# Performance work log

Measured on AMD Instinct MI355X. Metric: run time of the kernel, lower is better.

The kernel has to match this reference:

```python
import jax, jax.numpy as jnp
import numpy as np

N, E, F_IN, HID, C = 50000, 800000, 512, 256, 64
K, ALPHA = 10, 0.1


def setup_inputs() -> dict:
    key = jax.random.key(0)
    ks = jax.random.split(key, 6)
    x = jax.random.normal(ks[0], (N, F_IN), dtype=jnp.float32)
    edge_index = jax.random.randint(ks[1], (2, E), 0, N, dtype=jnp.int64)
    W1 = jax.random.normal(ks[2], (F_IN, HID), dtype=jnp.float32) / np.sqrt(F_IN)
    b1 = jnp.zeros((HID,), dtype=jnp.float32)
    W2 = jax.random.normal(ks[3], (HID, C), dtype=jnp.float32) / np.sqrt(HID)
    b2 = jnp.zeros((C,), dtype=jnp.float32)
    return {"x": x, "W1": W1, "b1": b1, "W2": W2, "b2": b2, "edge_index": edge_index}


def reference(x, W1, b1, W2, b2, edge_index):
    # MLP (dropout is identity in eval mode)
    h = jax.nn.relu(x @ W1 + b1)
    h = h @ W2 + b2  # [N, C]

    n = x.shape[0]
    self_loops = jnp.arange(n, dtype=edge_index.dtype)
    row = jnp.concatenate([edge_index[0], self_loops])  # source nodes
    col = jnp.concatenate([edge_index[1], self_loops])  # target nodes

    # GCN symmetric normalization with self-loops (PyG gcn_norm)
    deg = jax.ops.segment_sum(jnp.ones_like(col, dtype=h.dtype), col, num_segments=n)
    dinv = jnp.where(deg > 0, jax.lax.rsqrt(jnp.maximum(deg, 1e-12)), 0.0)
    norm = (dinv[row] * dinv[col])[:, None]  # [E+N, 1]

    x0 = h

    def step(z, _):
        msg = z[row] * norm                                    # gather + scale
        agg = jax.ops.segment_sum(msg, col, num_segments=n)    # scatter-add
        return (1.0 - ALPHA) * agg + ALPHA * x0, None

    z, _ = jax.lax.scan(step, x0, None, length=K)
    return z
```

## Files before the change

### kernel.cpp

```cpp
#include <hip/hip_runtime.h>

#define N_NODES 50000
#define N_EDGES 800000
#define F_INDIM 512
#define HID     256
#define N_CLS   64
#define K_STEPS 10
#define ALPHA_V 0.1f

#define NPB 28
#define NPW 7
#define ECAP 1536

typedef __attribute__((ext_vector_type(8))) short short8;
typedef __attribute__((ext_vector_type(4))) float f32x4;
typedef __attribute__((ext_vector_type(4))) unsigned short ushort4v;

__device__ __forceinline__ unsigned short f2bf(float f) {
  unsigned u = __builtin_bit_cast(unsigned, f);
  unsigned r = (u + 0x7fffu + ((u >> 16) & 1u)) >> 16;
  return (unsigned short)r;
}
__device__ __forceinline__ float bflo(unsigned g) {
  return __builtin_bit_cast(float, g << 16);
}
__device__ __forceinline__ float bfhi(unsigned g) {
  return __builtin_bit_cast(float, g & 0xffff0000u);
}

#define GLOAD_LDS16(g, l)                                                        \
  __builtin_amdgcn_global_load_lds(                                              \
      (const __attribute__((address_space(1))) unsigned int*)(g),                \
      (__attribute__((address_space(3))) unsigned int*)(l), 16, 0, 0)

__global__ void detect_kernel(const int* __restrict__ eb, int* __restrict__ flag) {
  __shared__ int any;
  if (threadIdx.x == 0) any = 0;
  __syncthreads();
  for (int j = threadIdx.x; j < 1024; j += 256) {
    if (eb[2 * j + 1] != 0) atomicOr(&any, 1);
  }
  __syncthreads();
  if (threadIdx.x == 0) flag[0] = any ? 0 : 1;
}

__global__ void count_kernel(const int* __restrict__ eb, const int* __restrict__ flagp,
                             int* __restrict__ cnt) {
  int e = blockIdx.x * 256 + threadIdx.x;
  if (e >= N_EDGES) return;
  int sh = flagp[0];
  int c = eb[((size_t)(N_EDGES + e)) << sh];
  atomicAdd(&cnt[c], 1);
}

__global__ void scan1_kernel(const int* __restrict__ cnt, int* __restrict__ ptr,
                             int* __restrict__ bsum) {
  __shared__ int sm[256];
  int t = threadIdx.x;
  int i = blockIdx.x * 256 + t;
  int v = (i < N_NODES) ? cnt[i] : 0;
  sm[t] = v;
  __syncthreads();
  for (int off = 1; off < 256; off <<= 1) {
    int x = sm[t];
    if (t >= off) x += sm[t - off];
    __syncthreads();
    sm[t] = x;
    __syncthreads();
  }
  int incl = sm[t];
  if (i < N_NODES) ptr[i] = incl - v;
  if (t == 255) bsum[blockIdx.x] = incl;
}

__global__ void scan2_kernel(int* __restrict__ bsum, int nblk) {
  __shared__ int sm[256];
  int t = threadIdx.x;
  int v = (t < nblk) ? bsum[t] : 0;
  sm[t] = v;
  __syncthreads();
  for (int off = 1; off < 256; off <<= 1) {
    int x = sm[t];
    if (t >= off) x += sm[t - off];
    __syncthreads();
    sm[t] = x;
    __syncthreads();
  }
  int incl = sm[t];
  if (t < nblk) bsum[t] = incl - v;
}

__global__ void scan3_kernel(int* __restrict__ ptr, const int* __restrict__ bsum) {
  int i = blockIdx.x * 256 + threadIdx.x;
  if (i < N_NODES) ptr[i] += bsum[i >> 8];
  if (i == 0) ptr[N_NODES] = N_EDGES;
}

__global__ void dinv_kernel(const int* __restrict__ cnt, const int* __restrict__ ptr,
                            float* __restrict__ dinv, float* __restrict__ selfw,
                            int* __restrict__ cursor) {
  int i = blockIdx.x * 256 + threadIdx.x;
  if (i >= N_NODES) return;
  float di = rsqrtf((float)cnt[i] + 1.0f);
  dinv[i] = di;
  selfw[i] = (1.0f - ALPHA_V) * di * di;
  cursor[i] = ptr[i];
}

__global__ void fill_kernel(const int* __restrict__ eb, const int* __restrict__ flagp,
                            const float* __restrict__ dinv, int* __restrict__ cursor,
                            int2* __restrict__ epack) {
  int e = blockIdx.x * 256 + threadIdx.x;
  if (e >= N_EDGES) return;
  int sh = flagp[0];
  int r = eb[((size_t)e) << sh];
  int c = eb[((size_t)(N_EDGES + e)) << sh];
  int pos = atomicAdd(&cursor[c], 1);
  float w = (1.0f - ALPHA_V) * dinv[r] * dinv[c];
  epack[pos] = make_int2(r, __float_as_int(w));
}

__global__ void prep_w(const float* __restrict__ W1, const float* __restrict__ W2,
                       unsigned short* __restrict__ W1T, unsigned short* __restrict__ W2T) {
  int i = blockIdx.x * 256 + threadIdx.x;
  if (i < F_INDIM * HID) {
    int k = i >> 8, c = i & 255;
    W1T[(size_t)c * F_INDIM + k] = f2bf(W1[i]);
  }
  int j = i - F_INDIM * HID;
  if (j >= 0 && j < HID * N_CLS) {
    int k = j >> 6, c = j & 63;
    W2T[(size_t)c * HID + k] = f2bf(W2[j]);
  }
}

__global__ __launch_bounds__(256, 4) void gemm1_mfma(
    const float* __restrict__ A, const unsigned short* __restrict__ BT,
    const float* __restrict__ bias, unsigned short* __restrict__ H, int M) {
  __shared__ unsigned short Ab[2][64 * 32];
  __shared__ unsigned short Bb[2][256 * 32];
  const int t = threadIdx.x;
  const int wave = t >> 6, lane = t & 63;
  const int l15 = lane & 15, l4 = lane >> 4;
  const int row0 = blockIdx.x * 64;

  f32x4 acc[16];
#pragma unroll
  for (int n = 0; n < 16; ++n) acc[n] = (f32x4)0.0f;

  const int NT = F_INDIM / 32;

  auto stageB = [&](int buf, int kt) {
#pragma unroll
    for (int i = 0; i < 4; ++i) {
      int row = wave * 64 + i * 16 + (lane >> 2);
      int g = lane & 3;
      int kg = g ^ ((row >> 1) & 3);
      const unsigned short* src = BT + (size_t)row * F_INDIM + kt * 32 + kg * 8;
      unsigned short* dst = &Bb[buf][(wave * 64 + i * 16) * 32];
      GLOAD_LDS16(src, dst);
    }
  };
  f32x4 ar[2];
  int arow[2], acol[2];
  auto loadA = [&](int kt) {
#pragma unroll
    for (int i = 0; i < 2; ++i) {
      int idx = wave * 512 + i * 256 + lane * 4;
      int row = idx >> 5;
      int col = idx & 31;
      arow[i] = row; acol[i] = col;
      int gr = row0 + row;
      if (gr > M - 1) gr = M - 1;
      ar[i] = *(const f32x4*)(A + (size_t)gr * F_INDIM + kt * 32 + col);
    }
  };
  auto writeA = [&](int buf) {
#pragma unroll
    for (int i = 0; i < 2; ++i) {
      int row = arow[i], col = acol[i];
      int g = col >> 3;
      int gp = g ^ ((row >> 1) & 3);
      ushort4v o;
#pragma unroll
      for (int j = 0; j < 4; ++j) o[j] = f2bf(ar[i][j]);
      *(ushort4v*)(&Ab[buf][row * 32 + gp * 8 + (col & 7)]) = o;
    }
  };
  auto compute = [&](int buf) {
    int rowA = wave * 16 + l15;
    short8 af = *(const short8*)(&Ab[buf][rowA * 32 + (l4 ^ ((rowA >> 1) & 3)) * 8]);
#pragma unroll
    for (int n = 0; n < 16; ++n) {
      int c = n * 16 + l15;
      short8 bf = *(const short8*)(&Bb[buf][c * 32 + (l4 ^ ((c >> 1) & 3)) * 8]);
      acc[n] = __builtin_amdgcn_mfma_f32_16x16x32_bf16(af, bf, acc[n], 0, 0, 0);
    }
  };

  stageB(0, 0);
  loadA(0);
  writeA(0);
  __syncthreads();
#pragma unroll 4
  for (int kt = 0; kt < NT; ++kt) {
    int cur = kt & 1;
    if (kt + 1 < NT) {
      stageB(cur ^ 1, kt + 1);
      loadA(kt + 1);
    }
    compute(cur);
    if (kt + 1 < NT) writeA(cur ^ 1);
    __syncthreads();
  }

#pragma unroll
  for (int i = 0; i < 4; ++i) {
    int grow = row0 + wave * 16 + l4 * 4 + i;
    if (grow >= M) continue;
#pragma unroll
    for (int n = 0; n < 16; ++n) {
      int gcol = n * 16 + l15;
      float v = fmaxf(acc[n][i] + bias[gcol], 0.0f);
      H[(size_t)grow * HID + gcol] = f2bf(v);
    }
  }
}

__global__ __launch_bounds__(256) void gemm2_mfma(
    const unsigned short* __restrict__ Hm, const unsigned short* __restrict__ BT,
    const float* __restrict__ bias, unsigned short* __restrict__ Ch,
    int roff, int M) {
  const int t = threadIdx.x;
  const int wave = t >> 6, lane = t & 63;
  const int l15 = lane & 15, l4 = lane >> 4;
  const int row0 = blockIdx.x * 64 + wave * 16;

  f32x4 acc[4];
#pragma unroll
  for (int n = 0; n < 4; ++n) acc[n] = (f32x4)0.0f;

  int gr = row0 + l15;
  if (gr > M - 1) gr = M - 1;
  const unsigned short* arow = Hm + (size_t)gr * HID + l4 * 8;

#pragma unroll
  for (int kt = 0; kt < HID / 32; ++kt) {
    short8 af = *(const short8*)(arow + kt * 32);
    short8 bf[4];
#pragma unroll
    for (int n = 0; n < 4; ++n)
      bf[n] = *(const short8*)(BT + (size_t)(n * 16 + l15) * HID + kt * 32 + l4 * 8);
#pragma unroll
    for (int n = 0; n < 4; ++n)
      acc[n] = __builtin_amdgcn_mfma_f32_16x16x32_bf16(af, bf[n], acc[n], 0, 0, 0);
  }

#pragma unroll
  for (int n = 0; n < 4; ++n) {
    int gcol = n * 16 + l15;
    float bv = bias[gcol];
#pragma unroll
    for (int i = 0; i < 4; ++i) {
      int grow = row0 + l4 * 4 + i;
      if (grow < M) {
        float v = acc[n][i] + bv;
        Ch[(size_t)(roff + grow) * N_CLS + gcol] = f2bf(v);
      }
    }
  }
}

template <bool LAST>
__global__ __launch_bounds__(256) void prop_step(
    const unsigned int* __restrict__ zin, const unsigned int* __restrict__ x0h,
    const float* __restrict__ selfw, const int* __restrict__ ptr,
    const int2* __restrict__ epack, unsigned int* __restrict__ zout,
    float* __restrict__ outf) {
  __shared__ int2 erec[ECAP];
  __shared__ int lptr[NPB + 1];
  __shared__ float lsw[NPB];

  const int tid = threadIdx.x;
  const int n0 = blockIdx.x * NPB;
  int nEnd = N_NODES - n0;
  if (nEnd > NPB) nEnd = NPB;

  if (tid <= nEnd) lptr[tid] = ptr[n0 + tid];
  if (tid < nEnd) lsw[tid] = selfw[n0 + tid];
  __syncthreads();
  const int base = lptr[0];
  const int cnt = lptr[nEnd] - base;
  for (int i = tid; i < cnt && i < ECAP; i += 256) erec[i] = epack[base + i];
  __syncthreads();

  const int wv = tid >> 6, lane = tid & 63;
  const int half = lane >> 5, cl = lane & 31;

  auto run = [&](auto getrec) {
    for (int ni = wv * NPW; ni < wv * NPW + NPW; ++ni) {
      if (ni >= nEnd) break;
      const int node = n0 + ni;
      float a0 = 0.0f, a1 = 0.0f;
      if (half == 0) {
        unsigned zs = zin[(size_t)node * 32 + cl];
        unsigned xs = x0h[(size_t)node * 32 + cl];
        float sw = lsw[ni];
        a0 = fmaf(sw, bflo(zs), ALPHA_V * bflo(xs));
        a1 = fmaf(sw, bfhi(zs), ALPHA_V * bfhi(xs));
      }
      int e = lptr[ni] - base, e1 = lptr[ni + 1] - base;
      for (; e + 16 <= e1; e += 16) {
        int2 p[8];
#pragma unroll
        for (int j = 0; j < 8; ++j) p[j] = getrec(e + 2 * j + half);
        unsigned g[8];
#pragma unroll
        for (int j = 0; j < 8; ++j) g[j] = zin[(size_t)p[j].x * 32 + cl];
#pragma unroll
        for (int j = 0; j < 8; ++j) {
          float w = __int_as_float(p[j].y);
          a0 = fmaf(w, bflo(g[j]), a0);
          a1 = fmaf(w, bfhi(g[j]), a1);
        }
      }
      if (e < e1) {
        int2 p[8];
        float m[8];
#pragma unroll
        for (int j = 0; j < 8; ++j) {
          int gi = e + 2 * j + half;
          bool ok = gi < e1;
          p[j] = getrec(ok ? gi : e);
          m[j] = ok ? 1.0f : 0.0f;
        }
        unsigned g[8];
#pragma unroll
        for (int j = 0; j < 8; ++j) g[j] = zin[(size_t)p[j].x * 32 + cl];
#pragma unroll
        for (int j = 0; j < 8; ++j) {
          float w = m[j] * __int_as_float(p[j].y);
          a0 = fmaf(w, bflo(g[j]), a0);
          a1 = fmaf(w, bfhi(g[j]), a1);
        }
      }
      a0 += __shfl_xor(a0, 32);
      a1 += __shfl_xor(a1, 32);
      if (half == 0) {
        if (LAST) {
          *(float2*)(outf + (size_t)node * 64 + 2 * cl) = make_float2(a0, a1);
        } else {
          zout[(size_t)node * 32 + cl] =
              (unsigned)f2bf(a0) | ((unsigned)f2bf(a1) << 16);
        }
      }
    }
  };

  if (cnt <= ECAP) {
    run([&](int i) { return erec[i]; });
  } else {
    run([&](int i) { return epack[base + i]; });
  }
}

extern "C" void kernel_launch(void* const* d_in, const int* in_sizes, int n_in,
                              void* d_out, int out_size, void* d_ws, size_t ws_size,
                              hipStream_t stream) {
  const float* x  = (const float*)d_in[0];
  const float* W1 = (const float*)d_in[1];
  const float* b1 = (const float*)d_in[2];
  const float* W2 = (const float*)d_in[3];
  const float* b2 = (const float*)d_in[4];
  const int*   eb = (const int*)d_in[5];
  float* out = (float*)d_out;

  char* ws = (char*)d_ws;
  size_t off = 0;
  auto alloc = [&](size_t bytes) -> void* {
    void* p = ws + off;
    off = (off + bytes + 255) & ~(size_t)255;
    return p;
  };

  int*   flagp  = (int*)alloc(256);
  int*   cnt    = (int*)alloc(N_NODES * sizeof(int));
  int*   ptr    = (int*)alloc((N_NODES + 1) * sizeof(int));
  int*   cursor = (int*)alloc(N_NODES * sizeof(int));
  int*   bsum   = (int*)alloc(256 * sizeof(int));
  float* dinv   = (float*)alloc(N_NODES * sizeof(float));
  float* selfw  = (float*)alloc(N_NODES * sizeof(float));
  int2*  epack  = (int2*)alloc((size_t)N_EDGES * sizeof(int2));
  unsigned short* W1T = (unsigned short*)alloc((size_t)HID * F_INDIM * sizeof(unsigned short));
  unsigned short* W2T = (unsigned short*)alloc((size_t)N_CLS * HID * sizeof(unsigned short));
  unsigned int* x0h = (unsigned int*)alloc((size_t)N_NODES * 32 * sizeof(unsigned int));
  unsigned int* z1  = (unsigned int*)alloc((size_t)N_NODES * 32 * sizeof(unsigned int));
  unsigned int* z2  = (unsigned int*)alloc((size_t)N_NODES * 32 * sizeof(unsigned int));

  int nchunks = 1;
  while (nchunks < 16) {
    size_t hbytes = (size_t)(N_NODES / nchunks) * HID * sizeof(unsigned short);
    if (off + hbytes <= ws_size) break;
    nchunks <<= 1;
  }
  int Mc = N_NODES / nchunks;
  unsigned short* h = (unsigned short*)alloc((size_t)Mc * HID * sizeof(unsigned short));

  hipMemsetAsync(cnt, 0, N_NODES * sizeof(int), stream);
  detect_kernel<<<1, 256, 0, stream>>>(eb, flagp);
  count_kernel<<<(N_EDGES + 255) / 256, 256, 0, stream>>>(eb, flagp, cnt);
  int nblk = (N_NODES + 255) / 256;
  scan1_kernel<<<nblk, 256, 0, stream>>>(cnt, ptr, bsum);
  scan2_kernel<<<1, 256, 0, stream>>>(bsum, nblk);
  scan3_kernel<<<nblk, 256, 0, stream>>>(ptr, bsum);
  dinv_kernel<<<nblk, 256, 0, stream>>>(cnt, ptr, dinv, selfw, cursor);
  fill_kernel<<<(N_EDGES + 255) / 256, 256, 0, stream>>>(eb, flagp, dinv, cursor, epack);
  prep_w<<<(F_INDIM * HID + HID * N_CLS + 255) / 256, 256, 0, stream>>>(W1, W2, W1T, W2T);

  for (int ci = 0; ci < nchunks; ++ci) {
    const float* Achunk = x + (size_t)ci * Mc * F_INDIM;
    dim3 g1((Mc + 63) / 64);
    gemm1_mfma<<<g1, 256, 0, stream>>>(Achunk, W1T, b1, h, Mc);
    dim3 g2((Mc + 63) / 64);
    gemm2_mfma<<<g2, 256, 0, stream>>>(h, W2T, b2,
        (unsigned short*)x0h, ci * Mc, Mc);
  }

  int pgrid = (N_NODES + NPB - 1) / NPB;
  const unsigned int* zin = x0h;
  unsigned int* zo[2] = {z1, z2};
  for (int s = 0; s < K_STEPS - 1; ++s) {
    unsigned int* zout = zo[s & 1];
    prop_step<false><<<pgrid, 256, 0, stream>>>(zin, x0h, selfw, ptr, epack, zout, nullptr);
    zin = zout;
  }
  prop_step<true><<<pgrid, 256, 0, stream>>>(zin, x0h, selfw, ptr, epack, nullptr, out);
}
```

Before: 383.8 us.

## Split gemm1 columns across blocks and widen propagation gathers to 8 bytes

gemm1 now tiles the 256 output columns into two 128-column blocks via a second grid dimension, halving accumulators and B staging per block. The aim is more blocks, lower register and LDS pressure and higher occupancy, at the cost of reading and converting the fp32 A tile twice. It also batches the B fragment LDS loads ahead of the MFMAs and hoists the bias loads. The propagation kernel now has 16 lanes each gather 4 bf16 channels (uint2) while 4 edge groups run per wave, then reduces with two shuffle stages, trading wider gathers for more shuffle work.

```diff
diff --git a/kernel.cpp b/kernel.cpp
--- a/kernel.cpp
+++ b/kernel.cpp
@@ -138,26 +138,26 @@
     const float* __restrict__ A, const unsigned short* __restrict__ BT,
     const float* __restrict__ bias, unsigned short* __restrict__ H, int M) {
   __shared__ unsigned short Ab[2][64 * 32];
-  __shared__ unsigned short Bb[2][256 * 32];
+  __shared__ unsigned short Bb[2][128 * 32];
   const int t = threadIdx.x;
   const int wave = t >> 6, lane = t & 63;
   const int l15 = lane & 15, l4 = lane >> 4;
-  const int row0 = blockIdx.x * 64;
-
-  f32x4 acc[16];
-#pragma unroll
-  for (int n = 0; n < 16; ++n) acc[n] = (f32x4)0.0f;
+  const int row0 = blockIdx.x * 64, col0 = blockIdx.y * 128;
+
+  f32x4 acc[8];
+#pragma unroll
+  for (int n = 0; n < 8; ++n) acc[n] = (f32x4)0.0f;
 
   const int NT = F_INDIM / 32;
 
   auto stageB = [&](int buf, int kt) {
 #pragma unroll
-    for (int i = 0; i < 4; ++i) {
-      int row = wave * 64 + i * 16 + (lane >> 2);
+    for (int i = 0; i < 2; ++i) {
+      int row = wave * 32 + i * 16 + (lane >> 2);
       int g = lane & 3;
       int kg = g ^ ((row >> 1) & 3);
-      const unsigned short* src = BT + (size_t)row * F_INDIM + kt * 32 + kg * 8;
-      unsigned short* dst = &Bb[buf][(wave * 64 + i * 16) * 32];
+      const unsigned short* src = BT + (size_t)(col0 + row) * F_INDIM + kt * 32 + kg * 8;
+      unsigned short* dst = &Bb[buf][(wave * 32 + i * 16) * 32];
       GLOAD_LDS16(src, dst);
     }
   };
@@ -190,12 +190,15 @@
   auto compute = [&](int buf) {
     int rowA = wave * 16 + l15;
     short8 af = *(const short8*)(&Ab[buf][rowA * 32 + (l4 ^ ((rowA >> 1) & 3)) * 8]);
-#pragma unroll
-    for (int n = 0; n < 16; ++n) {
+    short8 bf[8];
+#pragma unroll
+    for (int n = 0; n < 8; ++n) {
       int c = n * 16 + l15;
-      short8 bf = *(const short8*)(&Bb[buf][c * 32 + (l4 ^ ((c >> 1) & 3)) * 8]);
-      acc[n] = __builtin_amdgcn_mfma_f32_16x16x32_bf16(af, bf, acc[n], 0, 0, 0);
-    }
+      bf[n] = *(const short8*)(&Bb[buf][c * 32 + (l4 ^ ((c >> 1) & 3)) * 8]);
+    }
+#pragma unroll
+    for (int n = 0; n < 8; ++n)
+      acc[n] = __builtin_amdgcn_mfma_f32_16x16x32_bf16(af, bf[n], acc[n], 0, 0, 0);
   };
 
   stageB(0, 0);
@@ -214,14 +217,17 @@
     __syncthreads();
   }
 
+  float bv[8];
+#pragma unroll
+  for (int n = 0; n < 8; ++n) bv[n] = bias[col0 + n * 16 + l15];
 #pragma unroll
   for (int i = 0; i < 4; ++i) {
     int grow = row0 + wave * 16 + l4 * 4 + i;
     if (grow >= M) continue;
 #pragma unroll
-    for (int n = 0; n < 16; ++n) {
-      int gcol = n * 16 + l15;
-      float v = fmaxf(acc[n][i] + bias[gcol], 0.0f);
+    for (int n = 0; n < 8; ++n) {
+      int gcol = col0 + n * 16 + l15;
+      float v = fmaxf(acc[n][i] + bv[n], 0.0f);
       H[(size_t)grow * HID + gcol] = f2bf(v);
     }
   }
@@ -295,63 +301,76 @@
   __syncthreads();
 
   const int wv = tid >> 6, lane = tid & 63;
-  const int half = lane >> 5, cl = lane & 31;
+  const int eg = lane >> 4, c4 = lane & 15;
 
   auto run = [&](auto getrec) {
     for (int ni = wv * NPW; ni < wv * NPW + NPW; ++ni) {
       if (ni >= nEnd) break;
       const int node = n0 + ni;
-      float a0 = 0.0f, a1 = 0.0f;
-      if (half == 0) {
-        unsigned zs = zin[(size_t)node * 32 + cl];
-        unsigned xs = x0h[(size_t)node * 32 + cl];
+      float a0 = 0.f, a1 = 0.f, a2 = 0.f, a3 = 0.f;
+      if (eg == 0) {
+        uint2 zs = *(const uint2*)&zin[(size_t)node * 32 + 2 * c4];
+        uint2 xs = *(const uint2*)&x0h[(size_t)node * 32 + 2 * c4];
         float sw = lsw[ni];
-        a0 = fmaf(sw, bflo(zs), ALPHA_V * bflo(xs));
-        a1 = fmaf(sw, bfhi(zs), ALPHA_V * bfhi(xs));
+        a0 = fmaf(sw, bflo(zs.x), ALPHA_V * bflo(xs.x));
+        a1 = fmaf(sw, bfhi(zs.x), ALPHA_V * bfhi(xs.x));
+        a2 = fmaf(sw, bflo(zs.y), ALPHA_V * bflo(xs.y));
+        a3 = fmaf(sw, bfhi(zs.y), ALPHA_V * bfhi(xs.y));
       }
       int e = lptr[ni] - base, e1 = lptr[ni + 1] - base;
       for (; e + 16 <= e1; e += 16) {
-        int2 p[8];
-#pragma unroll
-        for (int j = 0; j < 8; ++j) p[j] = getrec(e + 2 * j + half);
-        unsigned g[8];
-#pragma unroll
-        for (int j = 0; j < 8; ++j) g[j] = zin[(size_t)p[j].x * 32 + cl];
-#pragma unroll
-        for (int j = 0; j < 8; ++j) {
+        int2 p[4];
+#pragma unroll
+        for (int j = 0; j < 4; ++j) p[j] = getrec(e + 4 * j + eg);
+        uint2 g[4];
+#pragma unroll
+        for (int j = 0; j < 4; ++j)
+          g[j] = *(const uint2*)&zin[(size_t)p[j].x * 32 + 2 * c4];
+#pragma unroll
+        for (int j = 0; j < 4; ++j) {
           float w = __int_as_float(p[j].y);
-          a0 = fmaf(w, bflo(g[j]), a0);
-          a1 = fmaf(w, bfhi(g[j]), a1);
+          a0 = fmaf(w, bflo(g[j].x), a0);
+          a1 = fmaf(w, bfhi(g[j].x), a1);
+          a2 = fmaf(w, bflo(g[j].y), a2);
+          a3 = fmaf(w, bfhi(g[j].y), a3);
         }
       }
       if (e < e1) {
-        int2 p[8];
-        float m[8];
-#pragma unroll
-        for (int j = 0; j < 8; ++j) {
-          int gi = e + 2 * j + half;
+        int2 p[4];
+        float m[4];
+#pragma unroll
+        for (int j = 0; j < 4; ++j) {
+          int gi = e + 4 * j + eg;
           bool ok = gi < e1;
           p[j] = getrec(ok ? gi : e);
           m[j] = ok ? 1.0f : 0.0f;
         }
-        unsigned g[8];
-#pragma unroll
-        for (int j = 0; j < 8; ++j) g[j] = zin[(size_t)p[j].x * 32 + cl];
-#pragma unroll
-        for (int j = 0; j < 8; ++j) {
+        uint2 g[4];
+#pragma unroll
+        for (int j = 0; j < 4; ++j)
+          g[j] = *(const uint2*)&zin[(size_t)p[j].x * 32 + 2 * c4];
+#pragma unroll
+        for (int j = 0; j < 4; ++j) {
           float w = m[j] * __int_as_float(p[j].y);
-          a0 = fmaf(w, bflo(g[j]), a0);
-          a1 = fmaf(w, bfhi(g[j]), a1);
+          a0 = fmaf(w, bflo(g[j].x), a0);
+          a1 = fmaf(w, bfhi(g[j].x), a1);
+          a2 = fmaf(w, bflo(g[j].y), a2);
+          a3 = fmaf(w, bfhi(g[j].y), a3);
         }
       }
-      a0 += __shfl_xor(a0, 32);
-      a1 += __shfl_xor(a1, 32);
-      if (half == 0) {
+      a0 += __shfl_xor(a0, 16); a0 += __shfl_xor(a0, 32);
+      a1 += __shfl_xor(a1, 16); a1 += __shfl_xor(a1, 32);
+      a2 += __shfl_xor(a2, 16); a2 += __shfl_xor(a2, 32);
+      a3 += __shfl_xor(a3, 16); a3 += __shfl_xor(a3, 32);
+      if (eg == 0) {
         if (LAST) {
-          *(float2*)(outf + (size_t)node * 64 + 2 * cl) = make_float2(a0, a1);
+          *(float4*)(outf + (size_t)node * 64 + 4 * c4) =
+              make_float4(a0, a1, a2, a3);
         } else {
-          zout[(size_t)node * 32 + cl] =
-              (unsigned)f2bf(a0) | ((unsigned)f2bf(a1) << 16);
+          uint2 o;
+          o.x = (unsigned)f2bf(a0) | ((unsigned)f2bf(a1) << 16);
+          o.y = (unsigned)f2bf(a2) | ((unsigned)f2bf(a3) << 16);
+          *(uint2*)&zout[(size_t)node * 32 + 2 * c4] = o;
         }
       }
     }
@@ -419,7 +438,7 @@
 
   for (int ci = 0; ci < nchunks; ++ci) {
     const float* Achunk = x + (size_t)ci * Mc * F_INDIM;
-    dim3 g1((Mc + 63) / 64);
+    dim3 g1((Mc + 63) / 64, HID / 128);
     gemm1_mfma<<<g1, 256, 0, stream>>>(Achunk, W1T, b1, h, Mc);
     dim3 g2((Mc + 63) / 64);
     gemm2_mfma<<<g2, 256, 0, stream>>>(h, W2T, b2,
```

After: 358.2 us. 6.7% less time.
